# Performance work log

Measured on AMD Instinct MI355X. Metric: run time of the kernel, lower is better.

Reference implementation:

```python
import jax, jax.numpy as jnp
import numpy as np

B, S, HID = 2, 2048, 2048
H, HK, D = 32, 8, 64
N_REP = H // HK
SCALE = D ** -0.5


def setup_inputs() -> dict:
    key = jax.random.key(0)
    ks = jax.random.split(key, 9)
    std = HID ** -0.5
    causal = jnp.tril(jnp.ones((S, S), dtype=bool))
    attention_mask = jnp.where(causal, 0.0, -1e9).astype(jnp.float32)[None, None]  # [1,1,S,S]
    return {
        "hidden_states": jax.random.normal(ks[0], (B, S, HID), jnp.float32),
        "attention_mask": attention_mask,
        "q_w": jax.random.normal(ks[1], (HID, H * D), jnp.float32) * std,
        "q_b": jax.random.normal(ks[2], (H * D,), jnp.float32) * 0.01,
        "k_w": jax.random.normal(ks[3], (HID, HK * D), jnp.float32) * std,
        "k_b": jax.random.normal(ks[4], (HK * D,), jnp.float32) * 0.01,
        "v_w": jax.random.normal(ks[5], (HID, HK * D), jnp.float32) * std,
        "v_b": jax.random.normal(ks[6], (HK * D,), jnp.float32) * 0.01,
        "dense_w": jax.random.normal(ks[7], (HID, HID), jnp.float32) * std,
        "dense_b": jax.random.normal(ks[8], (HID,), jnp.float32) * 0.01,
    }


def reference(hidden_states, attention_mask, q_w, q_b, k_w, k_b, v_w, v_b, dense_w, dense_b):
    b, s, _ = hidden_states.shape
    # projections -> [b, h, s, d]
    q = (hidden_states @ q_w + q_b).reshape(b, s, H, D).transpose(0, 2, 1, 3)
    k = (hidden_states @ k_w + k_b).reshape(b, s, HK, D).transpose(0, 2, 1, 3)
    v = (hidden_states @ v_w + v_b).reshape(b, s, HK, D).transpose(0, 2, 1, 3)
    # GQA: repeat_kv (repeat_interleave along head dim)
    k = jnp.repeat(k, N_REP, axis=1)  # [b, H, s, d]
    v = jnp.repeat(v, N_REP, axis=1)
    # eager attention: full score matrix
    scores = jnp.einsum("bhqd,bhkd->bhqk", q, k) * SCALE + attention_mask
    w = jax.nn.softmax(scores.astype(jnp.float32), axis=-1).astype(q.dtype)
    attn = jnp.einsum("bhqk,bhkd->bhqd", w, v)
    attn = attn.transpose(0, 2, 1, 3).reshape(b, s, H * D)
    return attn @ dense_w + dense_b
```

## Files before the change

kernel.cpp:

```cpp
#include <hip/hip_runtime.h>
#include <hip/hip_bf16.h>


typedef short s16x8 __attribute__((ext_vector_type(8)));
typedef float f32x4 __attribute__((ext_vector_type(4)));

static constexpr int BB = 2, SS = 2048, HID = 2048, HH = 32, HKV = 8, DD = 64;
static constexpr int MM = BB * SS;
static constexpr int NQKV = 3072;

#define DEV __device__ __forceinline__

DEV short f2bf(float f) {
    unsigned u = __builtin_bit_cast(unsigned, f);
    return (short)((u + 0x7fffu + ((u >> 16) & 1u)) >> 16);
}

DEV unsigned cvtpk(float lo, float hi) {
    unsigned r;
    asm("v_cvt_pk_bf16_f32 %0, %1, %2" : "=v"(r) : "v"(lo), "v"(hi));
    return r;
}

DEV void stage16(const short* gsrc, short* lbase) {
    __builtin_amdgcn_global_load_lds((const __attribute__((address_space(1))) void*)gsrc,
                                     (__attribute__((address_space(3))) void*)lbase, 16, 0, 0);
}

__global__ __launch_bounds__(256) void cvt_f32_bf16(const float* __restrict__ in,
                                                    short* __restrict__ out, int n) {
    int i = (blockIdx.x * 256 + threadIdx.x) * 8;
    if (i >= n) return;
    float4 a = *reinterpret_cast<const float4*>(in + i);
    float4 b = *reinterpret_cast<const float4*>(in + i + 4);
    s16x8 o;
    o[0] = f2bf(a.x); o[1] = f2bf(a.y); o[2] = f2bf(a.z); o[3] = f2bf(a.w);
    o[4] = f2bf(b.x); o[5] = f2bf(b.y); o[6] = f2bf(b.z); o[7] = f2bf(b.w);
    *reinterpret_cast<s16x8*>(out + i) = o;
}

__global__ __launch_bounds__(256) void transpose_cvt2(const float* __restrict__ in0,
                                                      short* __restrict__ out0,
                                                      const float* __restrict__ in1,
                                                      short* __restrict__ out1,
                                                      int K, int N) {
    __shared__ float tile[32][33];
    const float* in = blockIdx.z ? in1 : in0;
    short* out = blockIdx.z ? out1 : out0;
    int k0 = blockIdx.x * 32, n0 = blockIdx.y * 32;
    int tx = threadIdx.x & 31, ty = threadIdx.x >> 5;
#pragma unroll
    for (int r = ty; r < 32; r += 8)
        tile[r][tx] = in[(size_t)(k0 + r) * N + n0 + tx];
    __syncthreads();
#pragma unroll
    for (int r = ty; r < 32; r += 8)
        out[(size_t)(n0 + r) * K + k0 + tx] = f2bf(tile[tx][r]);
}

__global__ __launch_bounds__(256) void transpose_v(const short* __restrict__ QKV,
                                                   short* __restrict__ Vtg) {
    __shared__ int tile[32][33];
    const int s0 = blockIdx.x * 32, c0 = blockIdx.y * 32, b = blockIdx.z;
    const int tx = threadIdx.x & 31, ty = threadIdx.x >> 5;
#pragma unroll
    for (int r = ty; r < 32; r += 8)
        tile[r][tx] = QKV[(size_t)(b * SS + s0 + r) * NQKV + 2560 + c0 + tx];
    __syncthreads();
#pragma unroll
    for (int r = ty; r < 32; r += 8) {
        const int c = c0 + r;
        Vtg[((size_t)(b * HKV + (c >> 6)) * 64 + (c & 63)) * SS + s0 + tx] = (short)tile[tx][r];
    }
}

__global__ __launch_bounds__(256) void concat_bias(const float* __restrict__ qb,
                                                   const float* __restrict__ kb,
                                                   const float* __restrict__ vb,
                                                   float* __restrict__ cb) {
    int i = blockIdx.x * 256 + threadIdx.x;
    if (i < 2048) cb[i] = qb[i];
    else if (i < 2560) cb[i] = kb[i - 2048];
    else if (i < 3072) cb[i] = vb[i - 2560];
}

template <int BM, int BN, typename OutT>
__global__ __launch_bounds__(512) void gemm8p(const short* __restrict__ A,
                                              const short* __restrict__ Bt,
                                              const float* __restrict__ bias,
                                              OutT* __restrict__ C,
                                              int M, int N, int K, int qcols) {
    constexpr int NR = BN / 64;
    constexpr int ACH = BM * 4;
    constexpr int BCH = BN * 4;
    static_assert(ACH % 512 == 0, "A chunks per half must be thread-uniform");
    constexpr int SA = ACH / 512;
    __shared__ __align__(16) short lds[(BM + BN) * 128];
    const int tid = threadIdx.x, lane = tid & 63, wid = tid >> 6;
    const int fr = lane & 15, fk = lane >> 4;
    const int wm = wid >> 2, wn = wid & 3;
    const int nbn = N / BN;
    const int cpx = gridDim.x >> 3;
    const int wg = (blockIdx.x & 7) * cpx + (blockIdx.x >> 3);
    const int bm = wg / nbn, bn = wg % nbn;
    const int NT = K / 64;

    const short* Ablk = A + (size_t)bm * BM * K;
    const short* Bblk = Bt + (size_t)bn * BN * K;

    auto abase = [&](int bf, int kh) { return bf * (BM * 64) + kh * (BM * 32); };
    auto bbase = [&](int bf, int kh) { return 2 * (BM * 64) + bf * (BN * 64) + kh * (BN * 32); };

    auto stA = [&](int bf, int kh, int kt) {
#pragma unroll
        for (int l = 0; l < SA; ++l) {
            const int c = l * 512 + tid;
            const int r = c >> 2, sg = (c & 3) ^ ((r >> 1) & 3);
            stage16(Ablk + (size_t)r * K + kt + kh * 32 + sg * 8,
                    &lds[abase(bf, kh) + (l * 512 + wid * 64) * 8]);
        }
    };
    auto stB = [&](int bf, int kh, int kt) {
        {
            const int c = tid;
            const int r = c >> 2, sg = (c & 3) ^ ((r >> 1) & 3);
            stage16(Bblk + (size_t)r * K + kt + kh * 32 + sg * 8,
                    &lds[bbase(bf, kh) + (wid * 64) * 8]);
        }
        if constexpr (BCH > 512) {
            if (tid < BCH - 512) {
                const int c = 512 + tid;
                const int r = c >> 2, sg = (c & 3) ^ ((r >> 1) & 3);
                stage16(Bblk + (size_t)r * K + kt + kh * 32 + sg * 8,
                        &lds[bbase(bf, kh) + ((512 + wid * 64)) * 8]);
            }
        }
    };

    auto waithalf = [&](bool pf) {
        if (!pf) { asm volatile("s_waitcnt vmcnt(0)" ::: "memory"); return; }
        if constexpr (BCH > 512) {
            if (wid < (BCH - 512) / 64) asm volatile("s_waitcnt vmcnt(4)" ::: "memory");
            else                        asm volatile("s_waitcnt vmcnt(3)" ::: "memory");
        } else {
            asm volatile("s_waitcnt vmcnt(3)" ::: "memory");
        }
    };

    f32x4 acc[8][NR] = {};

    stA(0, 0, 0); stB(0, 0, 0);
    stA(0, 1, 0); stB(0, 1, 0);
    waithalf(true);
    asm volatile("s_barrier" ::: "memory");

    for (int t = 0; t < NT; ++t) {
        const int bf = t & 1, sf = bf ^ 1;
        const int ktn = (t + 1) * 64;
        const bool pf = (t + 1 < NT);
#pragma unroll
        for (int kh = 0; kh < 2; ++kh) {
            s16x8 bfrag[NR], afrag[8];
#pragma unroll
            for (int n = 0; n < NR; ++n) {
                const int row = wn * (BN / 4) + n * 16 + fr;
                bfrag[n] = *reinterpret_cast<const s16x8*>(
                    &lds[bbase(bf, kh) + row * 32 + ((fk ^ ((row >> 1) & 3)) * 8)]);
            }
#pragma unroll
            for (int i = 0; i < 8; ++i) {
                const int row = wm * 128 + i * 16 + fr;
                afrag[i] = *reinterpret_cast<const s16x8*>(
                    &lds[abase(bf, kh) + row * 32 + ((fk ^ ((row >> 1) & 3)) * 8)]);
            }
            if (pf) stA(sf, kh, ktn);
            __builtin_amdgcn_s_setprio(1);
#pragma unroll
            for (int i = 0; i < 4; ++i)
#pragma unroll
                for (int n = 0; n < NR; ++n)
                    acc[i][n] = __builtin_amdgcn_mfma_f32_16x16x32_bf16(
                        afrag[i], bfrag[n], acc[i][n], 0, 0, 0);
            __builtin_amdgcn_s_setprio(0);
            if (pf) stB(sf, kh, ktn);
            __builtin_amdgcn_s_setprio(1);
#pragma unroll
            for (int i = 4; i < 8; ++i)
#pragma unroll
                for (int n = 0; n < NR; ++n)
                    acc[i][n] = __builtin_amdgcn_mfma_f32_16x16x32_bf16(
                        afrag[i], bfrag[n], acc[i][n], 0, 0, 0);
            __builtin_amdgcn_s_setprio(0);
            waithalf(pf);
            asm volatile("s_barrier" ::: "memory");
        }
    }

#pragma unroll
    for (int n = 0; n < NR; ++n) {
        const int col = bn * BN + wn * (BN / 4) + n * 16 + fr;
        const float bv = bias[col];
        const float sc = (col < qcols) ? 0.125f : 1.0f;
#pragma unroll
        for (int mi = 0; mi < 8; ++mi) {
            const int row0 = bm * BM + wm * 128 + mi * 16 + fk * 4;
#pragma unroll
            for (int r = 0; r < 4; ++r) {
                const float v = (acc[mi][n][r] + bv) * sc;
                if constexpr (sizeof(OutT) == 2)
                    reinterpret_cast<short*>(C)[(size_t)(row0 + r) * N + col] = f2bf(v);
                else
                    reinterpret_cast<float*>(C)[(size_t)(row0 + r) * N + col] = v;
            }
        }
    }
}

__global__ __launch_bounds__(256) void gemm128(const short* __restrict__ A,
                                               const short* __restrict__ Bt,
                                               const float* __restrict__ bias,
                                               float* __restrict__ C,
                                               int M, int N, int K) {
    __shared__ __align__(16) short lds[256 * 128];
    const int tid = threadIdx.x, lane = tid & 63, wid = tid >> 6;
    const int fr = lane & 15, fk = lane >> 4;
    const int wm = wid >> 1, wn = wid & 1;
    const int nbn = N / 128;
    const int cpx = gridDim.x >> 3;
    const int wg = (blockIdx.x & 7) * cpx + (blockIdx.x >> 3);
    const int bm = wg / nbn, bn = wg % nbn;
    const int NT = K / 64;

    const short* Ablk = A + (size_t)bm * 128 * K;
    const short* Bblk = Bt + (size_t)bn * 128 * K;

    auto abase = [&](int bf, int kh) { return bf * (128 * 64) + kh * (128 * 32); };
    auto bbase = [&](int bf, int kh) { return 2 * (128 * 64) + bf * (128 * 64) + kh * (128 * 32); };

    auto stA = [&](int bf, int kh, int kt) {
#pragma unroll
        for (int l = 0; l < 2; ++l) {
            const int c = l * 256 + tid;
            const int r = c >> 2, sg = (c & 3) ^ ((r >> 1) & 3);
            stage16(Ablk + (size_t)r * K + kt + kh * 32 + sg * 8,
                    &lds[abase(bf, kh) + (l * 256 + wid * 64) * 8]);
        }
    };
    auto stB = [&](int bf, int kh, int kt) {
#pragma unroll
        for (int l = 0; l < 2; ++l) {
            const int c = l * 256 + tid;
            const int r = c >> 2, sg = (c & 3) ^ ((r >> 1) & 3);
            stage16(Bblk + (size_t)r * K + kt + kh * 32 + sg * 8,
                    &lds[bbase(bf, kh) + (l * 256 + wid * 64) * 8]);
        }
    };
    auto waithalf = [&](bool pf) {
        if (pf) asm volatile("s_waitcnt vmcnt(4)" ::: "memory");
        else    asm volatile("s_waitcnt vmcnt(0)" ::: "memory");
    };

    f32x4 acc[4][4] = {};

    stA(0, 0, 0); stB(0, 0, 0);
    stA(0, 1, 0); stB(0, 1, 0);
    waithalf(true);
    asm volatile("s_barrier" ::: "memory");

    for (int t = 0; t < NT; ++t) {
        const int bf = t & 1, sf = bf ^ 1;
        const int ktn = (t + 1) * 64;
        const bool pf = (t + 1 < NT);
#pragma unroll
        for (int kh = 0; kh < 2; ++kh) {
            s16x8 bfrag[4], afrag[4];
#pragma unroll
            for (int n = 0; n < 4; ++n) {
                const int row = wn * 64 + n * 16 + fr;
                bfrag[n] = *reinterpret_cast<const s16x8*>(
                    &lds[bbase(bf, kh) + row * 32 + ((fk ^ ((row >> 1) & 3)) * 8)]);
            }
#pragma unroll
            for (int i = 0; i < 4; ++i) {
                const int row = wm * 64 + i * 16 + fr;
                afrag[i] = *reinterpret_cast<const s16x8*>(
                    &lds[abase(bf, kh) + row * 32 + ((fk ^ ((row >> 1) & 3)) * 8)]);
            }
            if (pf) stA(sf, kh, ktn);
            __builtin_amdgcn_s_setprio(1);
#pragma unroll
            for (int i = 0; i < 2; ++i)
#pragma unroll
                for (int n = 0; n < 4; ++n)
                    acc[i][n] = __builtin_amdgcn_mfma_f32_16x16x32_bf16(
                        afrag[i], bfrag[n], acc[i][n], 0, 0, 0);
            __builtin_amdgcn_s_setprio(0);
            if (pf) stB(sf, kh, ktn);
            __builtin_amdgcn_s_setprio(1);
#pragma unroll
            for (int i = 2; i < 4; ++i)
#pragma unroll
                for (int n = 0; n < 4; ++n)
                    acc[i][n] = __builtin_amdgcn_mfma_f32_16x16x32_bf16(
                        afrag[i], bfrag[n], acc[i][n], 0, 0, 0);
            __builtin_amdgcn_s_setprio(0);
            waithalf(pf);
            asm volatile("s_barrier" ::: "memory");
        }
    }

#pragma unroll
    for (int n = 0; n < 4; ++n) {
        const int col = bn * 128 + wn * 64 + n * 16 + fr;
        const float bv = bias[col];
#pragma unroll
        for (int mi = 0; mi < 4; ++mi) {
            const int row0 = bm * 128 + wm * 64 + mi * 16 + fk * 4;
#pragma unroll
            for (int r = 0; r < 4; ++r)
                C[(size_t)(row0 + r) * N + col] = acc[mi][n][r] + bv;
        }
    }
}

__global__ __launch_bounds__(256, 2) void attn_fwd(
        const short* __restrict__ QKV,
        const short* __restrict__ Vtg,
        short* __restrict__ Ob) {
    constexpr int KB = 64;
    __shared__ __align__(16) short Qs[128 * 64];
    __shared__ __align__(16) short Ks[2][KB * 64];
    __shared__ __align__(16) short Vt[2][64 * 64];
    __shared__ __align__(16) short Ps[128 * 64];

    const int pair = blockIdx.x;
    const int bh = blockIdx.y;
    const int b = bh >> 5, h = bh & 31;
    const int kvh = h >> 2;
    const int tid = threadIdx.x, lane = tid & 63, wid = tid >> 6;
    const int fr = lane & 15, fk = lane >> 4;
    const int wq0 = wid * 32;

    const short* kbase = QKV + (size_t)b * SS * NQKV + 2048 + kvh * DD;
    const short* vbase = Vtg + (size_t)(b * HKV + kvh) * 64 * SS;

    auto stageKV = [&](int bb, int kv0) {
#pragma unroll
        for (int is = 0; is < 2; ++is) {
            const int c = is * 256 + wid * 64 + lane;
            const int r = c >> 3, sg = (c & 7) ^ (r & 7);
            stage16(kbase + (size_t)(kv0 + r) * NQKV + sg * 8,
                    &Ks[bb][(is * 256 + wid * 64) * 8]);
            stage16(vbase + (size_t)r * SS + kv0 + sg * 8,
                    &Vt[bb][(is * 256 + wid * 64) * 8]);
        }
    };
    auto stageQ = [&](int q0) {
        const short* qbase = QKV + ((size_t)b * SS + q0) * NQKV + h * DD;
#pragma unroll
        for (int is = 0; is < 4; ++is) {
            const int c = is * 256 + wid * 64 + lane;
            const int r = c >> 3, sg = (c & 7) ^ (r & 7);
            stage16(qbase + (size_t)r * NQKV + sg * 8,
                    &Qs[(is * 256 + wid * 64) * 8]);
        }
    };

    s16x8 ones = {};
    if (fr == 0) {
#pragma unroll
        for (int e = 0; e < 8; ++e) ones[e] = (short)0x3F80;
    }

    int cur = 0;
    stageQ(pair * 128);
    stageKV(0, 0);

    for (int sidx = 0; sidx < 2; ++sidx) {
        const int strip = sidx ? (15 - pair) : pair;
        const int q0 = strip * 128;
        const size_t qrow0 = (size_t)b * SS + q0;
        const int nt = 2 * strip + 2;

        __syncthreads();

        s16x8 bq[2][2];
#pragma unroll
        for (int i = 0; i < 2; ++i)
#pragma unroll
            for (int ks = 0; ks < 2; ++ks) {
                const int row = wq0 + i * 16 + fr;
                const int byte = (ks * 64 + fk * 16) ^ ((row & 7) << 4);
                bq[i][ks] = *reinterpret_cast<const s16x8*>(
                    reinterpret_cast<const char*>(Qs) + row * 128 + byte);
            }

        f32x4 acc_o[2][4] = {};
        f32x4 acc_l[2] = {};

        for (int t = 0; t < nt; ++t) {
            const int kv0 = t * KB;
            if (t + 1 < nt) {
                stageKV(cur ^ 1, kv0 + KB);
            } else if (sidx == 0) {
                stageQ((15 - pair) * 128);
                stageKV(cur ^ 1, 0);
            }

            f32x4 sacc[2][4] = {};
            __builtin_amdgcn_s_setprio(1);
#pragma unroll
            for (int j = 0; j < 4; ++j)
#pragma unroll
                for (int ks = 0; ks < 2; ++ks) {
                    const int row = j * 16 + fr;
                    const int byte = (ks * 64 + fk * 16) ^ ((row & 7) << 4);
                    s16x8 kf = *reinterpret_cast<const s16x8*>(
                        reinterpret_cast<const char*>(Ks[cur]) + row * 128 + byte);
#pragma unroll
                    for (int i = 0; i < 2; ++i)
                        sacc[i][j] = __builtin_amdgcn_mfma_f32_16x16x32_bf16(kf, bq[i][ks], sacc[i][j], 0, 0, 0);
                }
            __builtin_amdgcn_s_setprio(0);

            if (kv0 + KB - 1 > q0 + wq0) {
#pragma unroll
                for (int i = 0; i < 2; ++i) {
                    const int qg = q0 + wq0 + i * 16 + fr;
#pragma unroll
                    for (int j = 0; j < 4; ++j) {
                        const int kvb = kv0 + j * 16 + fk * 4;
#pragma unroll
                        for (int r = 0; r < 4; ++r)
                            if (kvb + r > qg) sacc[i][j][r] = -INFINITY;
                    }
                }
            }

#pragma unroll
            for (int i = 0; i < 2; ++i) {
                char* pbase = reinterpret_cast<char*>(Ps) + (wq0 + i * 16 + fr) * 128;
#pragma unroll
                for (int j = 0; j < 4; ++j)
#pragma unroll
                    for (int hh = 0; hh < 2; ++hh) {
                        const unsigned pw = cvtpk(__expf(sacc[i][j][2 * hh]),
                                                  __expf(sacc[i][j][2 * hh + 1]));
                        const int byte = ((j * 8 + fk * 2 + hh) << 2) ^ ((fr & 7) << 4);
                        *reinterpret_cast<unsigned*>(pbase + byte) = pw;
                    }
            }

            s16x8 ap[2][2];
#pragma unroll
            for (int i = 0; i < 2; ++i) {
                const char* pbase = reinterpret_cast<const char*>(Ps) + (wq0 + i * 16 + fr) * 128;
#pragma unroll
                for (int ks = 0; ks < 2; ++ks) {
                    const int byte = ((ks * 4 + fk) * 16) ^ ((fr & 7) << 4);
                    ap[i][ks] = *reinterpret_cast<const s16x8*>(pbase + byte);
                }
            }

            __builtin_amdgcn_s_setprio(1);
#pragma unroll
            for (int jd = 0; jd < 4; ++jd)
#pragma unroll
                for (int ks = 0; ks < 2; ++ks) {
                    const int row = jd * 16 + fr;
                    const int byte = (ks * 64 + fk * 16) ^ ((row & 7) << 4);
                    s16x8 bv = *reinterpret_cast<const s16x8*>(
                        reinterpret_cast<const char*>(Vt[cur]) + row * 128 + byte);
#pragma unroll
                    for (int i = 0; i < 2; ++i)
                        acc_o[i][jd] = __builtin_amdgcn_mfma_f32_16x16x32_bf16(ap[i][ks], bv, acc_o[i][jd], 0, 0, 0);
                }
#pragma unroll
            for (int i = 0; i < 2; ++i)
#pragma unroll
                for (int ks = 0; ks < 2; ++ks)
                    acc_l[i] = __builtin_amdgcn_mfma_f32_16x16x32_bf16(ap[i][ks], ones, acc_l[i], 0, 0, 0);
            __builtin_amdgcn_s_setprio(0);

            __syncthreads();
            cur ^= 1;
        }

#pragma unroll
        for (int i = 0; i < 2; ++i)
#pragma unroll
            for (int r = 0; r < 4; ++r) {
                const float l = __shfl(acc_l[i][r], (lane & 48));
                const float inv = 1.f / l;
                const size_t grow = (qrow0 + wq0 + i * 16 + fk * 4 + r) * (size_t)(HH * DD) + h * DD;
#pragma unroll
                for (int jd = 0; jd < 4; ++jd)
                    Ob[grow + jd * 16 + fr] = f2bf(acc_o[i][jd][r] * inv);
            }
    }
}

extern "C" void kernel_launch(void* const* d_in, const int* in_sizes, int n_in,
                              void* d_out, int out_size, void* d_ws, size_t ws_size,
                              hipStream_t stream) {
    const float* hidden  = (const float*)d_in[0];
    const float* q_w     = (const float*)d_in[2];
    const float* q_b     = (const float*)d_in[3];
    const float* k_w     = (const float*)d_in[4];
    const float* k_b     = (const float*)d_in[5];
    const float* v_w     = (const float*)d_in[6];
    const float* v_b     = (const float*)d_in[7];
    const float* dense_w = (const float*)d_in[8];
    const float* dense_b = (const float*)d_in[9];
    float* out = (float*)d_out;

    short* wt   = (short*)d_ws;
    short* dwt  = wt + 6291456;
    short* QKV  = dwt + 4194304;
    short* Vtg  = QKV + 12582912;
    short* hidb = Vtg + 2097152;
    short* Ob   = hidb;
    float* cbias = (float*)(hidb + 8388608);

    cvt_f32_bf16<<<4096, 256, 0, stream>>>(hidden, hidb, MM * HID);
    transpose_cvt2<<<dim3(64, 64, 2), 256, 0, stream>>>(q_w, wt, dense_w, dwt, HID, HID);
    transpose_cvt2<<<dim3(64, 16, 2), 256, 0, stream>>>(k_w, wt + 2048 * 2048,
                                                        v_w, wt + 2560 * 2048, HID, HKV * DD);
    concat_bias<<<12, 256, 0, stream>>>(q_b, k_b, v_b, cbias);

    gemm8p<256, 192, short><<<256, 512, 0, stream>>>(hidb, wt, cbias, QKV, MM, NQKV, HID, 2048);

    transpose_v<<<dim3(64, 16, 2), 256, 0, stream>>>(QKV, Vtg);

    attn_fwd<<<dim3(8, 64), 256, 0, stream>>>(QKV, Vtg, Ob);

    gemm128<<<512, 256, 0, stream>>>(Ob, dwt, dense_b, out, MM, HID, HID);
}
```

Baseline: 177.3 us.

## Shrink QKV GEMM tile to 128x192 with 256 threads; fold log2e into Q scale

Replaces the 256x192, 512-thread QKV projection GEMM with a 128x192 tile run by 256 threads, launching 512 workgroups instead of 256. This is meant to fill more compute units and spread the work more evenly, at the cost of less data reuse per tile. Q is now pre-scaled by 0.125·log2(e), so the attention softmax can call exp2f instead of __expf. That drops a multiply from each exponential, provided the max-subtraction code not shown here is consistent with base-2 scaling.

```diff
diff --git a/kernel.cpp b/kernel.cpp
--- a/kernel.cpp
+++ b/kernel.cpp
@@ -8,6 +8,7 @@
 static constexpr int BB = 2, SS = 2048, HID = 2048, HH = 32, HKV = 8, DD = 64;
 static constexpr int MM = BB * SS;
 static constexpr int NQKV = 3072;
+static constexpr float QSCALE = 0.18033688011112042f;
 
 #define DEV __device__ __forceinline__
 
@@ -84,21 +85,16 @@
     else if (i < 3072) cb[i] = vb[i - 2560];
 }
 
-template <int BM, int BN, typename OutT>
-__global__ __launch_bounds__(512) void gemm8p(const short* __restrict__ A,
-                                              const short* __restrict__ Bt,
-                                              const float* __restrict__ bias,
-                                              OutT* __restrict__ C,
-                                              int M, int N, int K, int qcols) {
-    constexpr int NR = BN / 64;
-    constexpr int ACH = BM * 4;
-    constexpr int BCH = BN * 4;
-    static_assert(ACH % 512 == 0, "A chunks per half must be thread-uniform");
-    constexpr int SA = ACH / 512;
+__global__ __launch_bounds__(256) void gemm_qkv(const short* __restrict__ A,
+                                                const short* __restrict__ Bt,
+                                                const float* __restrict__ bias,
+                                                short* __restrict__ C,
+                                                int M, int N, int K, int qcols) {
+    constexpr int BM = 128, BN = 192;
     __shared__ __align__(16) short lds[(BM + BN) * 128];
     const int tid = threadIdx.x, lane = tid & 63, wid = tid >> 6;
     const int fr = lane & 15, fk = lane >> 4;
-    const int wm = wid >> 2, wn = wid & 3;
+    const int wm = wid >> 1, wn = wid & 1;
     const int nbn = N / BN;
     const int cpx = gridDim.x >> 3;
     const int wg = (blockIdx.x & 7) * cpx + (blockIdx.x >> 3);
@@ -113,41 +109,28 @@
 
     auto stA = [&](int bf, int kh, int kt) {
 #pragma unroll
-        for (int l = 0; l < SA; ++l) {
-            const int c = l * 512 + tid;
+        for (int l = 0; l < 2; ++l) {
+            const int c = l * 256 + tid;
             const int r = c >> 2, sg = (c & 3) ^ ((r >> 1) & 3);
             stage16(Ablk + (size_t)r * K + kt + kh * 32 + sg * 8,
-                    &lds[abase(bf, kh) + (l * 512 + wid * 64) * 8]);
+                    &lds[abase(bf, kh) + (l * 256 + wid * 64) * 8]);
         }
     };
     auto stB = [&](int bf, int kh, int kt) {
-        {
-            const int c = tid;
+#pragma unroll
+        for (int l = 0; l < 3; ++l) {
+            const int c = l * 256 + tid;
             const int r = c >> 2, sg = (c & 3) ^ ((r >> 1) & 3);
             stage16(Bblk + (size_t)r * K + kt + kh * 32 + sg * 8,
-                    &lds[bbase(bf, kh) + (wid * 64) * 8]);
-        }
-        if constexpr (BCH > 512) {
-            if (tid < BCH - 512) {
-                const int c = 512 + tid;
-                const int r = c >> 2, sg = (c & 3) ^ ((r >> 1) & 3);
-                stage16(Bblk + (size_t)r * K + kt + kh * 32 + sg * 8,
-                        &lds[bbase(bf, kh) + ((512 + wid * 64)) * 8]);
-            }
-        }
-    };
-
+                    &lds[bbase(bf, kh) + (l * 256 + wid * 64) * 8]);
+        }
+    };
     auto waithalf = [&](bool pf) {
-        if (!pf) { asm volatile("s_waitcnt vmcnt(0)" ::: "memory"); return; }
-        if constexpr (BCH > 512) {
-            if (wid < (BCH - 512) / 64) asm volatile("s_waitcnt vmcnt(4)" ::: "memory");
-            else                        asm volatile("s_waitcnt vmcnt(3)" ::: "memory");
-        } else {
-            asm volatile("s_waitcnt vmcnt(3)" ::: "memory");
-        }
-    };
-
-    f32x4 acc[8][NR] = {};
+        if (pf) asm volatile("s_waitcnt vmcnt(5)" ::: "memory");
+        else    asm volatile("s_waitcnt vmcnt(0)" ::: "memory");
+    };
+
+    f32x4 acc[4][6] = {};
 
     stA(0, 0, 0); stB(0, 0, 0);
     stA(0, 1, 0); stB(0, 1, 0);
@@ -160,34 +143,34 @@
         const bool pf = (t + 1 < NT);
 #pragma unroll
         for (int kh = 0; kh < 2; ++kh) {
-            s16x8 bfrag[NR], afrag[8];
-#pragma unroll
-            for (int n = 0; n < NR; ++n) {
-                const int row = wn * (BN / 4) + n * 16 + fr;
+            s16x8 bfrag[6], afrag[4];
+#pragma unroll
+            for (int n = 0; n < 6; ++n) {
+                const int row = wn * 96 + n * 16 + fr;
                 bfrag[n] = *reinterpret_cast<const s16x8*>(
                     &lds[bbase(bf, kh) + row * 32 + ((fk ^ ((row >> 1) & 3)) * 8)]);
             }
 #pragma unroll
-            for (int i = 0; i < 8; ++i) {
-                const int row = wm * 128 + i * 16 + fr;
+            for (int i = 0; i < 4; ++i) {
+                const int row = wm * 64 + i * 16 + fr;
                 afrag[i] = *reinterpret_cast<const s16x8*>(
                     &lds[abase(bf, kh) + row * 32 + ((fk ^ ((row >> 1) & 3)) * 8)]);
             }
             if (pf) stA(sf, kh, ktn);
             __builtin_amdgcn_s_setprio(1);
 #pragma unroll
-            for (int i = 0; i < 4; ++i)
-#pragma unroll
-                for (int n = 0; n < NR; ++n)
+            for (int i = 0; i < 2; ++i)
+#pragma unroll
+                for (int n = 0; n < 6; ++n)
                     acc[i][n] = __builtin_amdgcn_mfma_f32_16x16x32_bf16(
                         afrag[i], bfrag[n], acc[i][n], 0, 0, 0);
             __builtin_amdgcn_s_setprio(0);
             if (pf) stB(sf, kh, ktn);
             __builtin_amdgcn_s_setprio(1);
 #pragma unroll
-            for (int i = 4; i < 8; ++i)
-#pragma unroll
-                for (int n = 0; n < NR; ++n)
+            for (int i = 2; i < 4; ++i)
+#pragma unroll
+                for (int n = 0; n < 6; ++n)
                     acc[i][n] = __builtin_amdgcn_mfma_f32_16x16x32_bf16(
                         afrag[i], bfrag[n], acc[i][n], 0, 0, 0);
             __builtin_amdgcn_s_setprio(0);
@@ -197,21 +180,16 @@
     }
 
 #pragma unroll
-    for (int n = 0; n < NR; ++n) {
-        const int col = bn * BN + wn * (BN / 4) + n * 16 + fr;
+    for (int n = 0; n < 6; ++n) {
+        const int col = bn * BN + wn * 96 + n * 16 + fr;
         const float bv = bias[col];
-        const float sc = (col < qcols) ? 0.125f : 1.0f;
-#pragma unroll
-        for (int mi = 0; mi < 8; ++mi) {
-            const int row0 = bm * BM + wm * 128 + mi * 16 + fk * 4;
-#pragma unroll
-            for (int r = 0; r < 4; ++r) {
-                const float v = (acc[mi][n][r] + bv) * sc;
-                if constexpr (sizeof(OutT) == 2)
-                    reinterpret_cast<short*>(C)[(size_t)(row0 + r) * N + col] = f2bf(v);
-                else
-                    reinterpret_cast<float*>(C)[(size_t)(row0 + r) * N + col] = v;
-            }
+        const float sc = (col < qcols) ? QSCALE : 1.0f;
+#pragma unroll
+        for (int mi = 0; mi < 4; ++mi) {
+            const int row0 = bm * BM + wm * 64 + mi * 16 + fk * 4;
+#pragma unroll
+            for (int r = 0; r < 4; ++r)
+                C[(size_t)(row0 + r) * N + col] = f2bf((acc[mi][n][r] + bv) * sc);
         }
     }
 }
@@ -444,8 +422,8 @@
                 for (int j = 0; j < 4; ++j)
 #pragma unroll
                     for (int hh = 0; hh < 2; ++hh) {
-                        const unsigned pw = cvtpk(__expf(sacc[i][j][2 * hh]),
-                                                  __expf(sacc[i][j][2 * hh + 1]));
+                        const unsigned pw = cvtpk(exp2f(sacc[i][j][2 * hh]),
+                                                  exp2f(sacc[i][j][2 * hh + 1]));
                         const int byte = ((j * 8 + fk * 2 + hh) << 2) ^ ((fr & 7) << 4);
                         *reinterpret_cast<unsigned*>(pbase + byte) = pw;
                     }
@@ -528,7 +506,7 @@
                                                         v_w, wt + 2560 * 2048, HID, HKV * DD);
     concat_bias<<<12, 256, 0, stream>>>(q_b, k_b, v_b, cbias);
 
-    gemm8p<256, 192, short><<<256, 512, 0, stream>>>(hidb, wt, cbias, QKV, MM, NQKV, HID, 2048);
+    gemm_qkv<<<512, 256, 0, stream>>>(hidb, wt, cbias, QKV, MM, NQKV, HID, 2048);
 
     transpose_v<<<dim3(64, 16, 2), 256, 0, stream>>>(QKV, Vtg);
 
```

Measured after the change: 192.9 us. 8.8% more time.
